# Kernel optimization log

Hardware: AMD Instinct MI355X
Metric: run time of the kernel (lower is better)

The kernel has to match this reference:

```python
import jax, jax.numpy as jnp
import numpy as np

T, B, S, H, E, V = 16, 32, 256, 256, 300, 1000


def setup_inputs() -> dict:
    key = jax.random.key(0)
    ks = jax.random.split(key, 16)
    p = lambda k, shp: (jax.random.normal(k, shp, dtype=jnp.float32) * 0.05)
    return {
        "target_variable": jax.random.randint(ks[0], (T, B), 0, V),
        "h0": p(ks[1], (1, B, H)),
        "c0": p(ks[2], (1, B, H)),
        "encoder_outputs": jax.random.normal(ks[3], (S, B, H), dtype=jnp.float32),
        "encoder_lens": jax.random.randint(ks[4], (B,), 1, S + 1),
        "embedding": p(ks[5], (V, E)),
        "W_ih": p(ks[6], (4 * H, E)),
        "W_hh": p(ks[7], (4 * H, H)),
        "b_ih": p(ks[8], (4 * H,)),
        "b_hh": p(ks[9], (4 * H,)),
        "We": p(ks[10], (H, H)),
        "be": p(ks[11], (H,)),
        "Wd": p(ks[12], (H, H)),
        "bd": p(ks[13], (H,)),
        "wa": p(ks[14], (H,)),
        "ba": p(ks[14], (1,)),
        "W_out": p(ks[15], (V, 2 * H)),
        "b_out": p(ks[15], (V,)),
    }


def _lstm(x, h0, c0, W_ih, W_hh, b_ih, b_hh):
    # x: [T,B,E]; torch gate order i,f,g,o
    x_proj = jnp.einsum('tbe,ge->tbg', x, W_ih) + b_ih  # [T,B,4H]
    def step(carry, xg):
        h, c = carry
        g = xg + h @ W_hh.T + b_hh
        i, f, gg, o = jnp.split(g, 4, axis=-1)
        c = jax.nn.sigmoid(f) * c + jax.nn.sigmoid(i) * jnp.tanh(gg)
        h = jax.nn.sigmoid(o) * jnp.tanh(c)
        return (h, c), h
    (hT, cT), outs = jax.lax.scan(step, (h0[0], c0[0]), x_proj)
    return outs, hT[None], cT[None]


def reference(target_variable, h0, c0, encoder_outputs, encoder_lens,
              embedding, W_ih, W_hh, b_ih, b_hh,
              We, be, Wd, bd, wa, ba, W_out, b_out):
    emb = embedding[target_variable]                      # [T,B,E] (dropout p=0 -> identity)
    output, hT, cT = _lstm(emb, h0, c0, W_ih, W_hh, b_ih, b_hh)  # output [T,B,H]
    # additive attention: same math as expand+Linear, applied before broadcast
    enc_t = jnp.einsum('sbh,gh->sbg', encoder_outputs, We) + be   # [S,B,H]
    dec_t = jnp.einsum('tbh,gh->tbg', output, Wd) + bd            # [T,B,H]
    scores = jnp.einsum('tsbh,h->tsb', jnp.tanh(enc_t[None, :, :, :] + dec_t[:, None, :, :]), wa) + ba[0]
    raw_attention = jnp.transpose(scores, (2, 0, 1))              # [B,T,S]
    valid = (jnp.arange(S)[None, None, :] < encoder_lens[:, None, None])  # [B,1,S]
    raw_attention = jnp.where(valid, raw_attention, -jnp.inf)
    attention = jax.nn.softmax(raw_attention, axis=2)             # [B,T,S]
    enc_bf = jnp.transpose(encoder_outputs, (1, 0, 2))            # [B,S,H]
    context = jnp.einsum('bts,bsh->bth', attention, enc_bf)       # [B,T,H]
    out_bf = jnp.transpose(output, (1, 0, 2))                     # [B,T,H]
    combined = jnp.transpose(jnp.concatenate([context, out_bf], axis=2), (1, 0, 2))  # [T,B,2H]
    logits = jnp.einsum('tbh,vh->tbv', combined, W_out) + b_out
    output_prob = jax.nn.softmax(logits, axis=2)                  # [T,B,V]
    return output_prob, hT, cT, context
```

## Files before the change

kernel.cpp:

```cpp
#include <hip/hip_runtime.h>
#include <hip/hip_fp16.h>
#include <math.h>

typedef unsigned int u32;
typedef unsigned short u16;

#define T_ 16
#define B_ 32
#define S_ 256
#define H_ 256
#define E_ 300
#define V_ 1000

typedef _Float16 h2_t __attribute__((ext_vector_type(2)));
typedef __fp16  fp16v2 __attribute__((ext_vector_type(2)));

__device__ __forceinline__ float fast_tanh(float x) {
    return 1.0f - 2.0f / (__expf(2.0f * x) + 1.0f);
}
__device__ __forceinline__ float fast_sigm(float x) {
    return 1.0f / (1.0f + __expf(-x));
}
__device__ __forceinline__ u32 pk2(float a, float b) {
    union { fp16v2 v; u32 u; } c; c.v = __builtin_amdgcn_cvt_pkrtz(a, b); return c.u;
}
__device__ __forceinline__ h2_t u2h2(u32 u) {
    union { u32 a; h2_t b; } c; c.a = u; return c.b;
}
__device__ __forceinline__ float dot2f16(u32 w, u32 h, float acc) {
#if __has_builtin(__builtin_amdgcn_fdot2)
    return __builtin_amdgcn_fdot2(u2h2(w), u2h2(h), acc, false);
#else
    h2_t wv = u2h2(w), hv = u2h2(h);
    return acc + (float)wv.x * (float)hv.x + (float)wv.y * (float)hv.y;
#endif
}

__global__ __launch_bounds__(256)
void prep_xproj(const float* __restrict__ emb, const int* __restrict__ tv,
                const float* __restrict__ W_ih, const float* __restrict__ b_ih,
                float* __restrict__ xproj,
                const float* __restrict__ Whh,  u32* __restrict__ Wt2)
{
    const int bid = blockIdx.x;
    const int tid = threadIdx.x;
    if (bid < 256) {
        __shared__ float As[32][33];
        __shared__ float Bs[32][64];
        const int bm = (bid >> 4) * 32;
        const int bn = (bid & 15) * 64;
        const int ty = tid >> 4;
        const int tx = tid & 15;
        const int alr = tid >> 3;
        const int alk = (tid & 7) * 4;
        const int blr = tid >> 2;
        const int blk = (tid & 3) * 8;

        const float* Ap = emb + (size_t)tv[bm + alr] * E_;
        const float* Bp = W_ih + (size_t)(bn + blr) * E_;

        float acc[2][4] = {};
        for (int k0 = 0; k0 < E_; k0 += 32) {
            int kb = k0 + alk;
            float4 a4;
            if (kb + 4 <= E_) {
                a4 = *(const float4*)(Ap + kb);
            } else {
                a4.x = (kb + 0 < E_) ? Ap[kb + 0] : 0.0f;
                a4.y = (kb + 1 < E_) ? Ap[kb + 1] : 0.0f;
                a4.z = (kb + 2 < E_) ? Ap[kb + 2] : 0.0f;
                a4.w = (kb + 3 < E_) ? Ap[kb + 3] : 0.0f;
            }
            As[alk + 0][alr] = a4.x; As[alk + 1][alr] = a4.y;
            As[alk + 2][alr] = a4.z; As[alk + 3][alr] = a4.w;

            int kbb = k0 + blk;
            float bv[8];
            if (kbb + 8 <= E_) {
                float4 p0 = *(const float4*)(Bp + kbb);
                float4 p1 = *(const float4*)(Bp + kbb + 4);
                bv[0]=p0.x; bv[1]=p0.y; bv[2]=p0.z; bv[3]=p0.w;
                bv[4]=p1.x; bv[5]=p1.y; bv[6]=p1.z; bv[7]=p1.w;
            } else {
                #pragma unroll
                for (int j = 0; j < 8; j++) bv[j] = (kbb + j < E_) ? Bp[kbb + j] : 0.0f;
            }
            #pragma unroll
            for (int j = 0; j < 8; j++) Bs[blk + j][blr] = bv[j];
            __syncthreads();
            #pragma unroll
            for (int kk = 0; kk < 32; kk++) {
                float ax = As[kk][ty * 2], ay = As[kk][ty * 2 + 1];
                float4 b = *(const float4*)&Bs[kk][tx * 4];
                acc[0][0] += ax*b.x; acc[0][1] += ax*b.y; acc[0][2] += ax*b.z; acc[0][3] += ax*b.w;
                acc[1][0] += ay*b.x; acc[1][1] += ay*b.y; acc[1][2] += ay*b.z; acc[1][3] += ay*b.w;
            }
            __syncthreads();
        }
        #pragma unroll
        for (int i = 0; i < 2; i++) {
            int m = bm + ty * 2 + i;
            #pragma unroll
            for (int j = 0; j < 4; j++) {
                int n = bn + tx * 4 + j;
                xproj[(size_t)m * 1024 + n] = acc[i][j] + b_ih[n];
            }
        }
        return;
    }
    __shared__ float tile[64][65];
    const int wv = tid >> 6;
    const int lane = tid & 63;
    int t = bid - 256;
    int r0 = (t >> 2) * 64, k0 = (t & 3) * 64;
    #pragma unroll 4
    for (int j = 0; j < 16; j++) {
        int row = wv * 16 + j;
        tile[row][lane] = Whh[(size_t)(r0 + row) * 256 + k0 + lane];
    }
    __syncthreads();
    #pragma unroll
    for (int it = 0; it < 2; it++) {
        int q = wv + 4 * it;
        uint4 val;
        val.x = pk2(tile[lane][8*q + 0], tile[lane][8*q + 1]);
        val.y = pk2(tile[lane][8*q + 2], tile[lane][8*q + 3]);
        val.z = pk2(tile[lane][8*q + 4], tile[lane][8*q + 5]);
        val.w = pk2(tile[lane][8*q + 6], tile[lane][8*q + 7]);
        ((uint4*)Wt2)[(size_t)((k0 >> 3) + q) * 1024 + r0 + lane] = val;
    }
}

__global__ __launch_bounds__(1024)
__attribute__((amdgpu_waves_per_eu(4, 4)))
void lstm_enct(const float* __restrict__ xproj,
               const u32*   __restrict__ Wt2,
               const float* __restrict__ bhh,
               const float* __restrict__ h0, const float* __restrict__ c0,
               float* __restrict__ combined,
               float* __restrict__ hT, float* __restrict__ cT,
               const float* __restrict__ enc_raw,
               const float* __restrict__ We,
               const float* __restrict__ be,
               float* __restrict__ enct,
               const float* __restrict__ Wd,   float* __restrict__ Wdt,
               const float* __restrict__ W_out, u32* __restrict__ WoT2)
{
    const int bid = blockIdx.x;
    const int tid = threadIdx.x;
    __shared__ __align__(16) u32 smem[38272];

    if (bid < 32) {
        float* zs = (float*)smem;
        float* cs = (float*)(smem + 1024);
        u32*   hp = smem + 1280;
        u32*   wlds = smem + 1408;
        float* hsave = (float*)(smem + 34176);
        const int b = bid;
        const int r = tid;
        if (tid < 256) {
            float h0v = h0[b * 256 + tid];
            cs[tid] = c0[b * 256 + tid];
            float hpart = __shfl_xor(h0v, 1, 64);
            if (!(tid & 1)) hp[tid >> 1] = pk2(h0v, hpart);
        }
        const float bh = bhh[r];
        const uint4* wp4 = (const uint4*)Wt2 + r;

        uint4 wreg[20];
        #pragma unroll
        for (int j = 0; j < 20; j++) wreg[j] = wp4[(size_t)(12 + j) * 1024];
        #pragma unroll
        for (int j = 0; j < 8; j++) {
            uint4 w = wp4[(size_t)(4 + j) * 1024];
            wlds[(j * 4 + 0) * 1024 + r] = w.x;
            wlds[(j * 4 + 1) * 1024 + r] = w.y;
            wlds[(j * 4 + 2) * 1024 + r] = w.z;
            wlds[(j * 4 + 3) * 1024 + r] = w.w;
        }
        __syncthreads();

        for (int t = 0; t < T_; t++) {
            float xp = xproj[((size_t)t * B_ + b) * 1024 + r];
            float acc = 0.0f;
            const uint4* hp4 = (const uint4*)hp;
            #pragma unroll
            for (int i = 0; i < 4; i++) {
                uint4 hv = hp4[i];
                uint4 w  = wp4[(size_t)i * 1024];
                acc = dot2f16(w.x, hv.x, acc);
                acc = dot2f16(w.y, hv.y, acc);
                acc = dot2f16(w.z, hv.z, acc);
                acc = dot2f16(w.w, hv.w, acc);
            }
            #pragma unroll
            for (int j = 0; j < 8; j++) {
                uint4 hv = hp4[4 + j];
                u32 w0 = wlds[(j * 4 + 0) * 1024 + r];
                u32 w1 = wlds[(j * 4 + 1) * 1024 + r];
                u32 w2 = wlds[(j * 4 + 2) * 1024 + r];
                u32 w3 = wlds[(j * 4 + 3) * 1024 + r];
                acc = dot2f16(w0, hv.x, acc);
                acc = dot2f16(w1, hv.y, acc);
                acc = dot2f16(w2, hv.z, acc);
                acc = dot2f16(w3, hv.w, acc);
            }
            #pragma unroll
            for (int j = 0; j < 20; j++) {
                uint4 hv = hp4[12 + j];
                acc = dot2f16(wreg[j].x, hv.x, acc);
                acc = dot2f16(wreg[j].y, hv.y, acc);
                acc = dot2f16(wreg[j].z, hv.z, acc);
                acc = dot2f16(wreg[j].w, hv.w, acc);
            }
            zs[r] = xp + bh + acc;
            __syncthreads();

            if (tid < 256) {
                float ig = fast_sigm(zs[tid]);
                float fg = fast_sigm(zs[256 + tid]);
                float gg = fast_tanh(zs[512 + tid]);
                float og = fast_sigm(zs[768 + tid]);
                float c = fg * cs[tid] + ig * gg;
                float h = og * fast_tanh(c);
                cs[tid] = c;
                hsave[(t << 8) + tid] = h;
                float hpart = __shfl_xor(h, 1, 64);
                if (!(tid & 1)) hp[tid >> 1] = pk2(h, hpart);
            }
            __syncthreads();
        }

        #pragma unroll
        for (int i = 0; i < 4; i++) {
            int idx = tid + i * 1024;
            int t = idx >> 8, h = idx & 255;
            combined[((size_t)t * B_ + b) * 512 + 256 + h] = hsave[idx];
        }
        if (tid < 256) {
            hT[b * 256 + tid] = hsave[(15 << 8) + tid];
            cT[b * 256 + tid] = cs[tid];
        }
    } else if (bid < 160) {
        float (*As2)[132] = (float (*)[132])smem;
        float (*Bs2)[132] = (float (*)[132])(smem + 4224);
        const int tile = bid - 32;
        const int bm = (tile >> 1) * 128;
        const int bn = (tile & 1) * 128;
        const int tx = tid & 31, ty = tid >> 5;
        const int lr = tid >> 3;
        const int lk = (tid & 7) * 4;

        const float* Ap = enc_raw + (size_t)(bm + lr) * 256;
        const float* Bp = We + (size_t)(bn + lr) * 256;
        float acc[4][4] = {};

        for (int k0 = 0; k0 < 256; k0 += 32) {
            float4 a4 = *(const float4*)(Ap + k0 + lk);
            float4 b4 = *(const float4*)(Bp + k0 + lk);
            As2[lk + 0][lr] = a4.x; As2[lk + 1][lr] = a4.y;
            As2[lk + 2][lr] = a4.z; As2[lk + 3][lr] = a4.w;
            Bs2[lk + 0][lr] = b4.x; Bs2[lk + 1][lr] = b4.y;
            Bs2[lk + 2][lr] = b4.z; Bs2[lk + 3][lr] = b4.w;
            __syncthreads();
            #pragma unroll
            for (int kk = 0; kk < 32; kk++) {
                float4 a = *(const float4*)&As2[kk][ty * 4];
                float4 b = *(const float4*)&Bs2[kk][tx * 4];
                acc[0][0] += a.x*b.x; acc[0][1] += a.x*b.y; acc[0][2] += a.x*b.z; acc[0][3] += a.x*b.w;
                acc[1][0] += a.y*b.x; acc[1][1] += a.y*b.y; acc[1][2] += a.y*b.z; acc[1][3] += a.y*b.w;
                acc[2][0] += a.z*b.x; acc[2][1] += a.z*b.y; acc[2][2] += a.z*b.z; acc[2][3] += a.z*b.w;
                acc[3][0] += a.w*b.x; acc[3][1] += a.w*b.y; acc[3][2] += a.w*b.z; acc[3][3] += a.w*b.w;
            }
            __syncthreads();
        }
        #pragma unroll
        for (int i = 0; i < 4; i++) {
            int m = bm + ty * 4 + i;
            #pragma unroll
            for (int j = 0; j < 4; j++) {
                int n = bn + tx * 4 + j;
                enct[(size_t)m * 256 + n] = acc[i][j] + be[n];
            }
        }
    } else if (bid < 176) {
        float (*tile)[65] = (float (*)[65])smem;
        const int w = tid >> 6;
        const int lane = tid & 63;
        int t = bid - 160;
        int h0 = (t >> 2) * 64, k0 = (t & 3) * 64;
        #pragma unroll
        for (int j = 0; j < 4; j++) {
            int row = w * 4 + j;
            tile[row][lane] = Wd[(size_t)(h0 + row) * 256 + k0 + lane];
        }
        __syncthreads();
        {
            int q = w;
            float4 v;
            v.x = tile[lane][4*q + 0];
            v.y = tile[lane][4*q + 1];
            v.z = tile[lane][4*q + 2];
            v.w = tile[lane][4*q + 3];
            ((float4*)Wdt)[(size_t)((k0 >> 2) + q) * 256 + h0 + lane] = v;
        }
    } else {
        float (*tile)[65] = (float (*)[65])smem;
        const int w = tid >> 6;
        const int lane = tid & 63;
        int t = bid - 176;
        int v0 = (t >> 3) * 64, k0 = (t & 7) * 64;
        #pragma unroll
        for (int j = 0; j < 4; j++) {
            int row = w * 4 + j;
            int v = v0 + row;
            tile[row][lane] = (v < V_) ? W_out[(size_t)v * 512 + k0 + lane] : 0.0f;
        }
        __syncthreads();
        if (w < 8) {
            int q = w;
            int v = v0 + lane;
            if (v < V_) {
                uint4 val;
                val.x = pk2(tile[lane][8*q + 0], tile[lane][8*q + 1]);
                val.y = pk2(tile[lane][8*q + 2], tile[lane][8*q + 3]);
                val.z = pk2(tile[lane][8*q + 4], tile[lane][8*q + 5]);
                val.w = pk2(tile[lane][8*q + 6], tile[lane][8*q + 7]);
                ((uint4*)WoT2)[(size_t)((k0 >> 3) + q) * 1000 + v] = val;
            }
        }
    }
}

__global__ __launch_bounds__(512)
void attn_logits(const float* __restrict__ enct,
                 const float* __restrict__ combined_in,
                 const float* __restrict__ Wdt,
                 const float* __restrict__ bd,
                 const float* __restrict__ enc_raw,
                 const float* __restrict__ wa, const float* __restrict__ ba,
                 const int* __restrict__ lens,
                 const u32* __restrict__ WoT2,
                 const float* __restrict__ b_out,
                 float* __restrict__ ctx_out,
                 float* __restrict__ probs)
{
    const int bid = blockIdx.x;
    const int b = bid & 31;
    const int t = bid >> 5;
    const int tid = threadIdx.x;
    const int wv = tid >> 6, lane = tid & 63;
    __shared__ float ds[256], was[256], sc[256];
    __shared__ float crow[512];
    __shared__ float tmp2[512];
    __shared__ float lrow[1000];
    __shared__ float red[8], red2[8];
    __shared__ u32 crow_pk[256];

    if (tid < 256) {
        crow[256 + tid] = combined_in[((size_t)t * B_ + b) * 512 + 256 + tid];
        was[tid] = wa[tid];
    }
    const int len = lens[b];
    const float bav = ba[0];
    __syncthreads();

    {
        const int h   = tid & 255;
        const int kq0 = (tid >> 8) * 32;
        float acc = 0.0f;
        const float4* wp = (const float4*)Wdt + h;
        #pragma unroll 8
        for (int kq = kq0; kq < kq0 + 32; kq++) {
            float4 w = wp[(size_t)kq * 256];
            float4 c = *(const float4*)&crow[256 + kq * 4];
            acc += w.x * c.x;
            acc += w.y * c.y;
            acc += w.z * c.z;
            acc += w.w * c.w;
        }
        tmp2[tid] = acc;
    }
    __syncthreads();
    if (tid < 256) ds[tid] = bd[tid] + tmp2[tid] + tmp2[tid + 256];
    __syncthreads();

    {
        float c0 = 0.f, c1 = 0.f, c2 = 0.f, c3 = 0.f;
        if (wv < len) {
            const float* er = enct + ((size_t)wv * B_ + b) * 256;
            c0 = er[lane]; c1 = er[lane + 64]; c2 = er[lane + 128]; c3 = er[lane + 192];
        }
        for (int s = wv; s < len; s += 8) {
            int sn = s + 8;
            float n0 = 0.f, n1 = 0.f, n2 = 0.f, n3 = 0.f;
            if (sn < len) {
                const float* ern = enct + ((size_t)sn * B_ + b) * 256;
                n0 = ern[lane]; n1 = ern[lane + 64]; n2 = ern[lane + 128]; n3 = ern[lane + 192];
            }
            float sum = 0.0f;
            sum += fast_tanh(c0 + ds[lane]) * was[lane];
            sum += fast_tanh(c1 + ds[lane + 64]) * was[lane + 64];
            sum += fast_tanh(c2 + ds[lane + 128]) * was[lane + 128];
            sum += fast_tanh(c3 + ds[lane + 192]) * was[lane + 192];
            #pragma unroll
            for (int off = 32; off >= 1; off >>= 1) sum += __shfl_xor(sum, off, 64);
            if (lane == 0) sc[s] = sum + bav;
            c0 = n0; c1 = n1; c2 = n2; c3 = n3;
        }
    }
    __syncthreads();

    float x = (tid < len) ? sc[tid] : -INFINITY;
    float m = x;
    #pragma unroll
    for (int off = 32; off >= 1; off >>= 1) m = fmaxf(m, __shfl_xor(m, off, 64));
    if (lane == 0) red[wv] = m;
    __syncthreads();
    m = red[0];
    #pragma unroll
    for (int i = 1; i < 8; i++) m = fmaxf(m, red[i]);
    float e = __expf(x - m);
    float ssum = e;
    #pragma unroll
    for (int off = 32; off >= 1; off >>= 1) ssum += __shfl_xor(ssum, off, 64);
    if (lane == 0) red2[wv] = ssum;
    __syncthreads();
    ssum = red2[0] + red2[1] + red2[2] + red2[3] + red2[4] + red2[5] + red2[6] + red2[7];
    if (tid < 256) sc[tid] = e / ssum;
    __syncthreads();

    {
        const int h  = tid & 255;
        const int sg = tid >> 8;
        const int mid = (len + 1) >> 1;
        const int s0 = sg ? mid : 0;
        const int s1 = sg ? len : mid;
        float cacc = 0.0f;
        const float* eb = enc_raw + (size_t)b * 256 + h;
        #pragma unroll 8
        for (int s = s0; s < s1; s++) cacc += sc[s] * eb[(size_t)s * (B_ * H_)];
        tmp2[tid] = cacc;
    }
    __syncthreads();
    if (tid < 256) {
        float ctx = tmp2[tid] + tmp2[tid + 256];
        ctx_out[((size_t)b * T_ + t) * 256 + tid] = ctx;
        crow[tid] = ctx;
    }
    __syncthreads();
    if (tid < 256) crow_pk[tid] = pk2(crow[2 * tid], crow[2 * tid + 1]);
    __syncthreads();

    if (tid < 500) {
        const int v0 = tid * 2;
        float a0 = b_out[v0], a1 = b_out[v0 + 1];
        const uint4* wp = (const uint4*)WoT2 + v0;
        const uint4* hp4 = (const uint4*)crow_pk;
        #pragma unroll 8
        for (int kq = 0; kq < 64; kq++) {
            uint4 w0 = wp[(size_t)kq * 1000];
            uint4 w1 = wp[(size_t)kq * 1000 + 1];
            uint4 hv = hp4[kq];
            a0 = dot2f16(w0.x, hv.x, a0);
            a0 = dot2f16(w0.y, hv.y, a0);
            a0 = dot2f16(w0.z, hv.z, a0);
            a0 = dot2f16(w0.w, hv.w, a0);
            a1 = dot2f16(w1.x, hv.x, a1);
            a1 = dot2f16(w1.y, hv.y, a1);
            a1 = dot2f16(w1.z, hv.z, a1);
            a1 = dot2f16(w1.w, hv.w, a1);
        }
        lrow[v0] = a0;
        lrow[v0 + 1] = a1;
    }
    __syncthreads();

    float v0v = -INFINITY, v1v = -INFINITY;
    if (tid < 500) { v0v = lrow[tid * 2]; v1v = lrow[tid * 2 + 1]; }
    float mx = fmaxf(v0v, v1v);
    #pragma unroll
    for (int off = 32; off >= 1; off >>= 1) mx = fmaxf(mx, __shfl_xor(mx, off, 64));
    if (lane == 0) red[wv] = mx;
    __syncthreads();
    mx = red[0];
    #pragma unroll
    for (int i = 1; i < 8; i++) mx = fmaxf(mx, red[i]);
    float e0 = __expf(v0v - mx), e1 = __expf(v1v - mx);
    float s2 = e0 + e1;
    #pragma unroll
    for (int off = 32; off >= 1; off >>= 1) s2 += __shfl_xor(s2, off, 64);
    if (lane == 0) red2[wv] = s2;
    __syncthreads();
    s2 = red2[0] + red2[1] + red2[2] + red2[3] + red2[4] + red2[5] + red2[6] + red2[7];
    float inv = 1.0f / s2;
    if (tid < 500) {
        float2 pv = make_float2(e0 * inv, e1 * inv);
        *(float2*)&probs[((size_t)t * B_ + b) * V_ + tid * 2] = pv;
    }
}

extern "C" void kernel_launch(void* const* d_in, const int* in_sizes, int n_in,
                              void* d_out, int out_size, void* d_ws, size_t ws_size,
                              hipStream_t stream) {
    const int*   tv       = (const int*)d_in[0];
    const float* h0       = (const float*)d_in[1];
    const float* c0       = (const float*)d_in[2];
    const float* enc_raw  = (const float*)d_in[3];
    const int*   lens     = (const int*)d_in[4];
    const float* emb      = (const float*)d_in[5];
    const float* W_ih     = (const float*)d_in[6];
    const float* W_hh     = (const float*)d_in[7];
    const float* b_ih     = (const float*)d_in[8];
    const float* b_hh     = (const float*)d_in[9];
    const float* We       = (const float*)d_in[10];
    const float* be       = (const float*)d_in[11];
    const float* Wd       = (const float*)d_in[12];
    const float* bd       = (const float*)d_in[13];
    const float* wa       = (const float*)d_in[14];
    const float* ba       = (const float*)d_in[15];
    const float* W_out    = (const float*)d_in[16];
    const float* b_out    = (const float*)d_in[17];

    float* ws       = (float*)d_ws;
    float* enct     = ws;
    float* xproj    = ws + 2097152;
    float* Wdt      = ws + 2621440;
    u32*   WoT2     = (u32*)(ws + 2752512);
    float* combined = ws + 3264512;
    u32*   Wt2      = (u32*)(ws + 3526656);

    float* out      = (float*)d_out;
    float* probs    = out;
    float* hT       = out + 512000;
    float* cT       = out + 520192;
    float* ctx_out  = out + 528384;

    prep_xproj<<<320, 256, 0, stream>>>(emb, tv, W_ih, b_ih, xproj, W_hh, Wt2);
    lstm_enct<<<304, 1024, 0, stream>>>(xproj, Wt2, b_hh, h0, c0, combined, hT, cT,
                                        enc_raw, We, be, enct,
                                        Wd, Wdt, W_out, WoT2);
    attn_logits<<<512, 512, 0, stream>>>(enct, combined, Wdt, bd, enc_raw,
                                         wa, ba, lens, WoT2, b_out, ctx_out, probs);
}
```

Measured before the change: 208.8 us.

## Split vocab projection into separate kernel processing two rows per block

The output projection and softmax move out of the attention kernel into a new kernel. Each block there handles two (t,b) rows, so every W_out weight load feeds two dot products and global weight traffic is halved. The packed fp16 combined vector is passed between the kernels through workspace memory, reusing the xproj buffer. The cost is an extra kernel launch, a global round-trip for the packed vector, and half as many blocks in the vocab stage.

```diff
diff --git a/kernel.cpp b/kernel.cpp
--- a/kernel.cpp
+++ b/kernel.cpp
@@ -340,10 +340,8 @@
                  const float* __restrict__ enc_raw,
                  const float* __restrict__ wa, const float* __restrict__ ba,
                  const int* __restrict__ lens,
-                 const u32* __restrict__ WoT2,
-                 const float* __restrict__ b_out,
                  float* __restrict__ ctx_out,
-                 float* __restrict__ probs)
+                 u32* __restrict__ crow_pk_ws)
 {
     const int bid = blockIdx.x;
     const int b = bid & 31;
@@ -353,9 +351,7 @@
     __shared__ float ds[256], was[256], sc[256];
     __shared__ float crow[512];
     __shared__ float tmp2[512];
-    __shared__ float lrow[1000];
     __shared__ float red[8], red2[8];
-    __shared__ u32 crow_pk[256];
 
     if (tid < 256) {
         crow[256 + tid] = combined_in[((size_t)t * B_ + b) * 512 + 256 + tid];
@@ -449,54 +445,92 @@
         crow[tid] = ctx;
     }
     __syncthreads();
-    if (tid < 256) crow_pk[tid] = pk2(crow[2 * tid], crow[2 * tid + 1]);
+    if (tid < 256)
+        crow_pk_ws[(size_t)(t * B_ + b) * 256 + tid] = pk2(crow[2 * tid], crow[2 * tid + 1]);
+}
+
+__global__ __launch_bounds__(512)
+void vocab_probs(const u32* __restrict__ crow_pk_ws,
+                 const u32* __restrict__ WoT2,
+                 const float* __restrict__ b_out,
+                 float* __restrict__ probs)
+{
+    const int bid = blockIdx.x;
+    const int r0 = bid * 2;
+    const int tid = threadIdx.x;
+    const int wv = tid >> 6, lane = tid & 63;
+    __shared__ u32 pk[2][256];
+    __shared__ float lrow[2][1000];
+    __shared__ float red[8], red2[8];
+
+    {
+        int rr = tid >> 8, idx = tid & 255;
+        pk[rr][idx] = crow_pk_ws[(size_t)(r0 + rr) * 256 + idx];
+    }
     __syncthreads();
 
     if (tid < 500) {
         const int v0 = tid * 2;
-        float a0 = b_out[v0], a1 = b_out[v0 + 1];
-        const uint4* wp = (const uint4*)WoT2 + v0;
-        const uint4* hp4 = (const uint4*)crow_pk;
-        #pragma unroll 8
+        const float b0v = b_out[v0], b1v = b_out[v0 + 1];
+        float a00 = b0v, a01 = b1v;
+        float a10 = b0v, a11 = b1v;
+        const uint4* wp  = (const uint4*)WoT2 + v0;
+        const uint4* h0p = (const uint4*)pk[0];
+        const uint4* h1p = (const uint4*)pk[1];
+        #pragma unroll 4
         for (int kq = 0; kq < 64; kq++) {
             uint4 w0 = wp[(size_t)kq * 1000];
             uint4 w1 = wp[(size_t)kq * 1000 + 1];
-            uint4 hv = hp4[kq];
-            a0 = dot2f16(w0.x, hv.x, a0);
-            a0 = dot2f16(w0.y, hv.y, a0);
-            a0 = dot2f16(w0.z, hv.z, a0);
-            a0 = dot2f16(w0.w, hv.w, a0);
-            a1 = dot2f16(w1.x, hv.x, a1);
-            a1 = dot2f16(w1.y, hv.y, a1);
-            a1 = dot2f16(w1.z, hv.z, a1);
-            a1 = dot2f16(w1.w, hv.w, a1);
-        }
-        lrow[v0] = a0;
-        lrow[v0 + 1] = a1;
-    }
-    __syncthreads();
-
-    float v0v = -INFINITY, v1v = -INFINITY;
-    if (tid < 500) { v0v = lrow[tid * 2]; v1v = lrow[tid * 2 + 1]; }
-    float mx = fmaxf(v0v, v1v);
+            uint4 hv0 = h0p[kq];
+            uint4 hv1 = h1p[kq];
+            a00 = dot2f16(w0.x, hv0.x, a00);
+            a00 = dot2f16(w0.y, hv0.y, a00);
+            a00 = dot2f16(w0.z, hv0.z, a00);
+            a00 = dot2f16(w0.w, hv0.w, a00);
+            a01 = dot2f16(w1.x, hv0.x, a01);
+            a01 = dot2f16(w1.y, hv0.y, a01);
+            a01 = dot2f16(w1.z, hv0.z, a01);
+            a01 = dot2f16(w1.w, hv0.w, a01);
+            a10 = dot2f16(w0.x, hv1.x, a10);
+            a10 = dot2f16(w0.y, hv1.y, a10);
+            a10 = dot2f16(w0.z, hv1.z, a10);
+            a10 = dot2f16(w0.w, hv1.w, a10);
+            a11 = dot2f16(w1.x, hv1.x, a11);
+            a11 = dot2f16(w1.y, hv1.y, a11);
+            a11 = dot2f16(w1.z, hv1.z, a11);
+            a11 = dot2f16(w1.w, hv1.w, a11);
+        }
+        lrow[0][v0] = a00; lrow[0][v0 + 1] = a01;
+        lrow[1][v0] = a10; lrow[1][v0 + 1] = a11;
+    }
+    __syncthreads();
+
     #pragma unroll
-    for (int off = 32; off >= 1; off >>= 1) mx = fmaxf(mx, __shfl_xor(mx, off, 64));
-    if (lane == 0) red[wv] = mx;
-    __syncthreads();
-    mx = red[0];
-    #pragma unroll
-    for (int i = 1; i < 8; i++) mx = fmaxf(mx, red[i]);
-    float e0 = __expf(v0v - mx), e1 = __expf(v1v - mx);
-    float s2 = e0 + e1;
-    #pragma unroll
-    for (int off = 32; off >= 1; off >>= 1) s2 += __shfl_xor(s2, off, 64);
-    if (lane == 0) red2[wv] = s2;
-    __syncthreads();
-    s2 = red2[0] + red2[1] + red2[2] + red2[3] + red2[4] + red2[5] + red2[6] + red2[7];
-    float inv = 1.0f / s2;
-    if (tid < 500) {
-        float2 pv = make_float2(e0 * inv, e1 * inv);
-        *(float2*)&probs[((size_t)t * B_ + b) * V_ + tid * 2] = pv;
+    for (int ti = 0; ti < 2; ti++) {
+        const int row = r0 + ti;
+        float v0v = -INFINITY, v1v = -INFINITY;
+        if (tid < 500) { v0v = lrow[ti][tid * 2]; v1v = lrow[ti][tid * 2 + 1]; }
+        float mx = fmaxf(v0v, v1v);
+        #pragma unroll
+        for (int off = 32; off >= 1; off >>= 1) mx = fmaxf(mx, __shfl_xor(mx, off, 64));
+        if (lane == 0) red[wv] = mx;
+        __syncthreads();
+        mx = red[0];
+        #pragma unroll
+        for (int i = 1; i < 8; i++) mx = fmaxf(mx, red[i]);
+        float e0 = __expf(v0v - mx), e1 = __expf(v1v - mx);
+        float s2 = e0 + e1;
+        #pragma unroll
+        for (int off = 32; off >= 1; off >>= 1) s2 += __shfl_xor(s2, off, 64);
+        if (lane == 0) red2[wv] = s2;
+        __syncthreads();
+        s2 = red2[0] + red2[1] + red2[2] + red2[3] + red2[4] + red2[5] + red2[6] + red2[7];
+        float inv = 1.0f / s2;
+        if (tid < 500) {
+            float2 pv = make_float2(e0 * inv, e1 * inv);
+            *(float2*)&probs[(size_t)row * V_ + tid * 2] = pv;
+        }
+        __syncthreads();
     }
 }
 
@@ -529,6 +563,7 @@
     u32*   WoT2     = (u32*)(ws + 2752512);
     float* combined = ws + 3264512;
     u32*   Wt2      = (u32*)(ws + 3526656);
+    u32*   crow_pk  = (u32*)xproj;
 
     float* out      = (float*)d_out;
     float* probs    = out;
@@ -541,5 +576,6 @@
                                         enc_raw, We, be, enct,
                                         Wd, Wdt, W_out, WoT2);
     attn_logits<<<512, 512, 0, stream>>>(enct, combined, Wdt, bd, enc_raw,
-                                         wa, ba, lens, WoT2, b_out, ctx_out, probs);
-}
+                                         wa, ba, lens, ctx_out, crow_pk);
+    vocab_probs<<<256, 512, 0, stream>>>(crow_pk, WoT2, b_out, probs);
+}
```

Result: no change. 206.5 us, median of 2 (-1.1%).
